# Optimization experiments

Measured on AMD Instinct MI355X. Metric: run time of the kernel, lower is better.

The kernel has to match this reference:

```python
import jax, jax.numpy as jnp
import numpy as np

DIM = 1024
SEQ_LEN = 4096
K_RANK = 256
HEADS = 16
HEAD_DIM = DIM // HEADS
BATCH = 4


def setup_inputs() -> dict:
    key = jax.random.key(0)
    k1, k2, k3, k4 = jax.random.split(key, 4)
    x = jax.random.normal(k1, (BATCH, SEQ_LEN, DIM), dtype=jnp.float32)
    W_qkv = jax.random.normal(k2, (DIM, 3 * DIM), dtype=jnp.float32) * (DIM ** -0.5)
    E = jax.random.normal(k3, (SEQ_LEN, K_RANK), dtype=jnp.float32)
    W_out = jax.random.normal(k4, (DIM, DIM), dtype=jnp.float32) * (DIM ** -0.5)
    b_out = jnp.zeros((DIM,), dtype=jnp.float32)
    return {"x": x, "W_qkv": W_qkv, "E": E, "W_out": W_out, "b_out": b_out}


def reference(x, W_qkv, E, W_out, b_out):
    B, N, D = x.shape
    scale = HEAD_DIM ** -0.5
    qkv = x @ W_qkv                                    # [B, N, 3D]
    q, k, v = jnp.split(qkv, 3, axis=-1)
    # [B, N, D] -> [B, H, N, hd]
    reshape_heads = lambda t: t.reshape(B, N, HEADS, HEAD_DIM).transpose(0, 2, 1, 3)
    q, k, v = map(reshape_heads, (q, k, v))
    # Linformer low-rank projection along sequence: [B, H, N, hd] -> [B, H, k, hd]
    k_proj = jnp.einsum('bhnd,nk->bhkd', k, E)
    v_proj = jnp.einsum('bhnd,nk->bhkd', v, E)
    scores = jnp.einsum('bhnd,bhkd->bhnk', q, k_proj) * scale  # [B, H, N, k]
    attn = jax.nn.softmax(scores, axis=-1)
    out = jnp.einsum('bhnk,bhkd->bhnd', attn, v_proj)  # [B, H, N, hd]
    out = out.transpose(0, 2, 1, 3).reshape(B, N, D)
    return out @ W_out + b_out
```

## Files before the change

### kernel.cpp

```cpp
#include <hip/hip_runtime.h>
#include <hip/hip_bf16.h>

typedef _Float16 f16;
typedef __attribute__((ext_vector_type(4))) _Float16 f16x4;
typedef __attribute__((ext_vector_type(8))) _Float16 f16x8;
typedef __attribute__((ext_vector_type(4))) float f32x4;

#define DIM 1024
#define SEQ 4096
#define KRNK 256
#define NH 16
#define HD 64
#define NB 4
#define ROWS (NB*SEQ)
#define NSPLIT 4

typedef const void __attribute__((address_space(1))) as1cv;
typedef void __attribute__((address_space(3))) as3v;

static __device__ __forceinline__ void glds16(const void* g, void* l) {
  __builtin_amdgcn_global_load_lds((as1cv*)g, (as3v*)l, 16, 0, 0);
}

template<int MODE>
__global__ __launch_bounds__(256) void k_prep_w(const float* __restrict__ in,
                                                f16* __restrict__ oh, f16* __restrict__ ol,
                                                int R, int C) {
  __shared__ float tile[64][65];
  int rtiles = R >> 6;
  int rt = blockIdx.x % rtiles, ct = blockIdx.x / rtiles;
  int r0 = rt << 6, c0 = ct << 6, t = threadIdx.x;
#pragma unroll
  for (int i = 0; i < 16; ++i) {
    int e = t + i * 256; int r = e >> 6, c = e & 63;
    tile[r][c] = in[(size_t)(r0 + r) * C + c0 + c];
  }
  __syncthreads();
#pragma unroll
  for (int i = 0; i < 16; ++i) {
    int e = t + i * 256; int c = e >> 6, r = e & 63;
    float v = tile[r][c];
    size_t idx = (size_t)(c0 + c) * R + r0 + r;
    if constexpr (MODE == 0) {
      v *= 256.0f;
      f16 h = (f16)v;
      oh[idx] = h;
      ol[idx] = (f16)(v - (float)h);
    } else {
      oh[idx] = (f16)v;
    }
  }
}

template<bool WH>
__global__ __launch_bounds__(256) void k_tsplit(const float* __restrict__ in,
                                                f16* __restrict__ oh,
                                                f16* __restrict__ oth,
                                                int R, int C) {
  __shared__ float tile[64][65];
  int rtiles = R >> 6;
  int rt = blockIdx.x % rtiles, ct = blockIdx.x / rtiles;
  int r0 = rt << 6, c0 = ct << 6, t = threadIdx.x;
  int cq = (t & 15) * 4, rr = t >> 4;
#pragma unroll
  for (int i = 0; i < 4; ++i) {
    int r = rr + i * 16;
    f32x4 v = *(const f32x4*)&in[(size_t)(r0 + r) * C + c0 + cq];
    tile[r][cq] = v[0]; tile[r][cq + 1] = v[1];
    tile[r][cq + 2] = v[2]; tile[r][cq + 3] = v[3];
    if constexpr (WH) {
      f16x4 h = {(f16)v[0], (f16)v[1], (f16)v[2], (f16)v[3]};
      *(f16x4*)&oh[(size_t)(r0 + r) * C + c0 + cq] = h;
    }
  }
  __syncthreads();
  int d4 = (t >> 4) * 4, sq = (t & 15) * 4;
#pragma unroll
  for (int j = 0; j < 4; ++j) {
    f16x4 h4;
#pragma unroll
    for (int k = 0; k < 4; ++k) h4[k] = (f16)tile[sq + k][d4 + j];
    *(f16x4*)&oth[(size_t)(c0 + d4 + j) * R + r0 + sq] = h4;
  }
}

template<bool ASPL, bool BSPL, int MT, int NT>
static __device__ __forceinline__ void mm_core(
    const f16* __restrict__ Ah, const f16* __restrict__ Al, int lda,
    const f16* __restrict__ Bh, const f16* __restrict__ Bl, int ldb,
    int bm, int bn, int K,
    f16* sAh, f16* sAl, f16* sBh, f16* sBl,
    f32x4 (&acc)[MT / 32][NT / 32]) {
  constexpr int MREP = MT / 32, NREP = NT / 32;
  constexpr int AI = MT / 32, BI = NT / 32;
  const int t = threadIdx.x;
  const int lane = t & 63, w = t >> 6;
  const int wr = w >> 1, wc = w & 1;
  const int l15 = lane & 15, hi = lane >> 4;
  const f32x4 zero = {0.f, 0.f, 0.f, 0.f};
#pragma unroll
  for (int m = 0; m < MREP; ++m)
#pragma unroll
    for (int n = 0; n < NREP; ++n) acc[m][n] = zero;

  for (int kk = 0; kk < K; kk += 64) {
#pragma unroll
    for (int i = 0; i < AI; ++i) {
      int c = t + i * 256;
      int row = c >> 3, cc = c & 7;
      size_t g = (size_t)(bm + row) * lda + kk + ((cc ^ (row & 7)) * 8);
      glds16(Ah + g, &sAh[c * 8]);
      if constexpr (ASPL) glds16(Al + g, &sAl[c * 8]);
    }
#pragma unroll
    for (int i = 0; i < BI; ++i) {
      int c = t + i * 256;
      int row = c >> 3, cc = c & 7;
      size_t g = (size_t)(bn + row) * ldb + kk + ((cc ^ (row & 7)) * 8);
      glds16(Bh + g, &sBh[c * 8]);
      if constexpr (BSPL) glds16(Bl + g, &sBl[c * 8]);
    }
    __syncthreads();

    f16x8 avh[MREP][2], avl[MREP][2], bvh[NREP][2], bvl[NREP][2];
#pragma unroll
    for (int m = 0; m < MREP; ++m)
#pragma unroll
      for (int ks = 0; ks < 2; ++ks) {
        int R = wr * (MT / 2) + m * 16 + l15;
        int off = R * 64 + (((ks * 4 + hi) ^ (R & 7)) * 8);
        avh[m][ks] = *(const f16x8*)&sAh[off];
        if constexpr (ASPL) avl[m][ks] = *(const f16x8*)&sAl[off];
      }
#pragma unroll
    for (int n = 0; n < NREP; ++n)
#pragma unroll
      for (int ks = 0; ks < 2; ++ks) {
        int R = wc * (NT / 2) + n * 16 + l15;
        int off = R * 64 + (((ks * 4 + hi) ^ (R & 7)) * 8);
        bvh[n][ks] = *(const f16x8*)&sBh[off];
        if constexpr (BSPL) bvl[n][ks] = *(const f16x8*)&sBl[off];
      }
#pragma unroll
    for (int m = 0; m < MREP; ++m)
#pragma unroll
      for (int n = 0; n < NREP; ++n)
#pragma unroll
        for (int ks = 0; ks < 2; ++ks) {
          if constexpr (ASPL && BSPL) {
            acc[m][n] = __builtin_amdgcn_mfma_f32_16x16x32_f16(avl[m][ks], bvh[n][ks], acc[m][n], 0, 0, 0);
            acc[m][n] = __builtin_amdgcn_mfma_f32_16x16x32_f16(avh[m][ks], bvl[n][ks], acc[m][n], 0, 0, 0);
          } else if constexpr (BSPL) {
            acc[m][n] = __builtin_amdgcn_mfma_f32_16x16x32_f16(avh[m][ks], bvl[n][ks], acc[m][n], 0, 0, 0);
          }
          acc[m][n] = __builtin_amdgcn_mfma_f32_16x16x32_f16(avh[m][ks], bvh[n][ks], acc[m][n], 0, 0, 0);
        }
    __syncthreads();
  }
}

__global__ __launch_bounds__(256) void k_xe2(const f16* __restrict__ Eth,
                                             const f16* __restrict__ xth,
                                             float* __restrict__ XEp) {
  __shared__ __align__(16) f16 sA[128 * 64];
  __shared__ __align__(16) f16 sB[64 * 64];
  int bx = blockIdx.x;
  int nt = bx & 15, mt = (bx >> 4) & 1, b = (bx >> 5) & 3, sp = bx >> 7;
  int bm = mt << 7, bn = nt << 6;
  int koff = sp * (SEQ / NSPLIT);
  f32x4 acc[4][2];
  mm_core<false, false, 128, 64>(Eth + koff, nullptr, SEQ,
                                 xth + (size_t)b * SEQ + koff, nullptr, ROWS,
                                 bm, bn, SEQ / NSPLIT, sA, nullptr, sB, nullptr, acc);
  const int t = threadIdx.x, lane = t & 63, w = t >> 6;
  const int wr = w >> 1, wc = w & 1, l15 = lane & 15, hi = lane >> 4;
#pragma unroll
  for (int m = 0; m < 4; ++m)
#pragma unroll
    for (int n = 0; n < 2; ++n)
#pragma unroll
      for (int r = 0; r < 4; ++r) {
        int kr = bm + wr * 64 + m * 16 + hi * 4 + r;
        int dd = bn + wc * 32 + n * 16 + l15;
        XEp[(((size_t)sp * NB + b) * KRNK + kr) * DIM + dd] = acc[m][n][r];
      }
}

__global__ __launch_bounds__(256) void k_xered(const float* __restrict__ XEp,
                                               f16* __restrict__ XEh,
                                               f16* __restrict__ XEl) {
  size_t i = (size_t)blockIdx.x * 256 + threadIdx.x;
  const size_t sstride = (size_t)NB * KRNK * DIM / 4;
  const f32x4* p = (const f32x4*)XEp;
  f32x4 s = p[i];
#pragma unroll
  for (int sp = 1; sp < NSPLIT; ++sp) s += p[i + sp * sstride];
  f16x4 h4, l4;
#pragma unroll
  for (int j = 0; j < 4; ++j) {
    f16 h = (f16)s[j];
    h4[j] = h;
    l4[j] = (f16)(s[j] - (float)h);
  }
  *(f16x4*)&XEh[i * 4] = h4;
  *(f16x4*)&XEl[i * 4] = l4;
}

__global__ __launch_bounds__(256) void k_gq(const f16* __restrict__ xh,
                                            const f16* __restrict__ Wph,
                                            f16* __restrict__ q) {
  __shared__ __align__(16) f16 sA[64 * 64];
  __shared__ __align__(16) f16 sB[128 * 64];
  int bx = blockIdx.x;
  int mt = bx & 255, nt = bx >> 8;
  int bm = mt << 6, bn = nt << 7;
  f32x4 acc[2][4];
  mm_core<false, false, 64, 128>(xh, nullptr, DIM, Wph, nullptr, DIM, bm, bn, DIM,
                                 sA, nullptr, sB, nullptr, acc);
  const int t = threadIdx.x, lane = t & 63, w = t >> 6;
  const int wr = w >> 1, wc = w & 1, l15 = lane & 15, hi = lane >> 4;
#pragma unroll
  for (int m = 0; m < 2; ++m)
#pragma unroll
    for (int n = 0; n < 4; ++n)
#pragma unroll
      for (int r = 0; r < 4; ++r) {
        int row = bm + wr * 32 + m * 16 + hi * 4 + r;
        int col = bn + wc * 64 + n * 16 + l15;
        q[(size_t)row * DIM + col] = (f16)(acc[m][n][r] * (1.0f / 256.0f));
      }
}

__global__ __launch_bounds__(256) void k_t2(const f16* __restrict__ XEh,
                                            const f16* __restrict__ XEl,
                                            const f16* __restrict__ Wph,
                                            const f16* __restrict__ Wpl,
                                            f16* __restrict__ kph,
                                            f16* __restrict__ vpt) {
  __shared__ __align__(16) f16 sAh[128 * 64], sAl[128 * 64];
  __shared__ __align__(16) f16 sBh[64 * 64], sBl[64 * 64];
  int bx = blockIdx.x;
  int nt = bx & 15, mt = (bx >> 4) & 1, b = (bx >> 5) & 3, kv = bx >> 7;
  size_t abase = (size_t)b * KRNK * DIM;
  size_t wbase = (size_t)(DIM + kv * DIM) * DIM;
  f32x4 acc[4][2];
  mm_core<true, true, 128, 64>(XEh + abase, XEl + abase, DIM, Wph + wbase, Wpl + wbase, DIM,
                               mt << 7, nt << 6, DIM, sAh, sAl, sBh, sBl, acc);
  const int t = threadIdx.x, lane = t & 63, w = t >> 6;
  const int wr = w >> 1, wc = w & 1, l15 = lane & 15, hi = lane >> 4;
#pragma unroll
  for (int m = 0; m < 4; ++m)
#pragma unroll
    for (int n = 0; n < 2; ++n)
#pragma unroll
      for (int r = 0; r < 4; ++r) {
        int row = (mt << 7) + wr * 64 + m * 16 + hi * 4 + r;
        int col = (nt << 6) + wc * 32 + n * 16 + l15;
        float s = acc[m][n][r] * (1.0f / 256.0f);
        if (!kv) kph[((size_t)(b * KRNK + row)) * DIM + col] = (f16)s;
        else     vpt[((size_t)(b * DIM + col)) * KRNK + row] = (f16)s;
      }
}

__global__ __launch_bounds__(256) void k_attn(const f16* __restrict__ q,
                                              const f16* __restrict__ kph,
                                              const f16* __restrict__ vpt,
                                              f16* __restrict__ oattn) {
  __shared__ __align__(16) f16 sBuf[2][64 * 64];
  __shared__ __align__(16) f16 sP[64 * KRNK];
  int bx0 = blockIdx.x;
  int swz = (bx0 & 7) * 512 + (bx0 >> 3);
  int qb = swz & 63;
  int bh = swz >> 6;
  int b = bh >> 4, h = bh & 15;
  int t = threadIdx.x;
  int lane = t & 63, w = t >> 6;
  int l15 = lane & 15, hi = lane >> 4;

  const f16* kbase = kph + ((size_t)(b * KRNK)) * DIM + h * HD;
  const f16* vbase = vpt + ((size_t)(b * DIM + h * HD)) * KRNK;

  auto stageK = [&](int c, int bufi) {
#pragma unroll
    for (int i = 0; i < 2; ++i) {
      int sid = w * 128 + i * 64 + lane;
      int kr = sid >> 3, sl = sid & 7;
      glds16(kbase + (size_t)(c * 64 + kr) * DIM + ((sl ^ (kr & 7)) * 8),
             &sBuf[bufi][sid * 8]);
    }
  };
  auto stageV = [&](int c, int bufi) {
#pragma unroll
    for (int i = 0; i < 2; ++i) {
      int sid = w * 128 + i * 64 + lane;
      int hd = sid >> 3, sl = sid & 7;
      glds16(vbase + (size_t)hd * KRNK + c * 64 + ((sl ^ (hd & 7)) * 8),
             &sBuf[bufi][sid * 8]);
    }
  };

  int seqrow = qb * 64 + w * 16 + l15;
  const f16* qg = q + ((size_t)(b * SEQ + seqrow)) * DIM + h * HD;
  f16x8 aq[2];
  aq[0] = *(const f16x8*)(qg + hi * 8);
  aq[1] = *(const f16x8*)(qg + 32 + hi * 8);

  const f32x4 zero = {0.f, 0.f, 0.f, 0.f};
  f32x4 s[16];

  stageK(0, 0);
#pragma unroll
  for (int c = 0; c < 4; ++c) {
    __syncthreads();
    if (c < 3) stageK(c + 1, (c + 1) & 1);
    else       stageV(0, 0);
#pragma unroll
    for (int n = 0; n < 4; ++n) {
      int nn = c * 4 + n;
      s[nn] = zero;
      int krl = n * 16 + l15;
#pragma unroll
      for (int ks = 0; ks < 2; ++ks) {
        f16x8 bk = *(const f16x8*)&sBuf[c & 1][krl * 64 + (((ks * 4 + hi) ^ (krl & 7)) * 8)];
        s[nn] = __builtin_amdgcn_mfma_f32_16x16x32_f16(bk, aq[ks], s[nn], 0, 0, 0);
      }
    }
  }

  const float scale = 0.125f;
  float m0 = s[0][0];
#pragma unroll
  for (int n = 0; n < 16; ++n)
#pragma unroll
    for (int r = 0; r < 4; ++r) m0 = fmaxf(m0, s[n][r]);
  m0 = fmaxf(m0, __shfl_xor(m0, 16));
  m0 = fmaxf(m0, __shfl_xor(m0, 32));
  float sm0 = 0.f, sm1 = 0.f, sm2 = 0.f, sm3 = 0.f;
#pragma unroll
  for (int n = 0; n < 16; ++n) {
    float p0 = __expf((s[n][0] - m0) * scale);
    float p1 = __expf((s[n][1] - m0) * scale);
    float p2 = __expf((s[n][2] - m0) * scale);
    float p3 = __expf((s[n][3] - m0) * scale);
    s[n][0] = p0; s[n][1] = p1; s[n][2] = p2; s[n][3] = p3;
    sm0 += p0; sm1 += p1; sm2 += p2; sm3 += p3;
  }
  float sm = (sm0 + sm1) + (sm2 + sm3);
  sm += __shfl_xor(sm, 16);
  sm += __shfl_xor(sm, 32);
  float inv = 1.0f / sm;

  {
    int qrow = w * 16 + l15;
    int qm = qrow & 7;
    f16* rowp = &sP[qrow * KRNK];
#pragma unroll
    for (int n = 0; n < 16; ++n) {
      int chunk = 2 * n + (hi >> 1);
      f16x4 pv = {(f16)s[n][0], (f16)s[n][1], (f16)s[n][2], (f16)s[n][3]};
      *(f16x4*)&rowp[((chunk ^ qm) * 8) + (hi & 1) * 4] = pv;
    }
  }

  f32x4 o[4];
#pragma unroll
  for (int n = 0; n < 4; ++n) o[n] = zero;
  int qloc = w * 16 + l15;
#pragma unroll
  for (int c = 0; c < 4; ++c) {
    __syncthreads();
    if (c < 3) stageV(c + 1, (c + 1) & 1);
#pragma unroll
    for (int sub = 0; sub < 2; ++sub) {
      int chunk = c * 8 + sub * 4 + hi;
      f16x8 pa = *(const f16x8*)&sP[qloc * KRNK + ((chunk ^ (qloc & 7)) * 8)];
#pragma unroll
      for (int n = 0; n < 4; ++n) {
        int hd = n * 16 + l15;
        f16x8 bv = *(const f16x8*)&sBuf[c & 1][hd * 64 + (((sub * 4 + hi) ^ (hd & 7)) * 8)];
        o[n] = __builtin_amdgcn_mfma_f32_16x16x32_f16(pa, bv, o[n], 0, 0, 0);
      }
    }
  }

  float invr[4];
#pragma unroll
  for (int r = 0; r < 4; ++r) invr[r] = __shfl(inv, hi * 4 + r);

  size_t obase = ((size_t)(b * SEQ + qb * 64)) * DIM + h * HD;
#pragma unroll
  for (int n = 0; n < 4; ++n)
#pragma unroll
    for (int r = 0; r < 4; ++r) {
      int qloc2 = w * 16 + hi * 4 + r;
      int hd = n * 16 + l15;
      oattn[obase + (size_t)qloc2 * DIM + hd] = (f16)(o[n][r] * invr[r]);
    }
}

__global__ __launch_bounds__(256) void k_go(const f16* __restrict__ oattn,
                                            const f16* __restrict__ WoT,
                                            const float* __restrict__ bias,
                                            float* __restrict__ out) {
  __shared__ __align__(16) f16 sA[128 * 64];
  __shared__ __align__(16) f16 sB[128 * 64];
  int bx = blockIdx.x;
  int mt = bx & 127, nt = bx >> 7;
  int bm = mt << 7, bn = nt << 7;
  f32x4 acc[4][4];
  mm_core<false, false, 128, 128>(oattn, nullptr, DIM, WoT, nullptr, DIM, bm, bn, DIM,
                                  sA, nullptr, sB, nullptr, acc);
  const int t = threadIdx.x, lane = t & 63, w = t >> 6;
  const int wr = w >> 1, wc = w & 1, l15 = lane & 15, hi = lane >> 4;
#pragma unroll
  for (int m = 0; m < 4; ++m)
#pragma unroll
    for (int n = 0; n < 4; ++n)
#pragma unroll
      for (int r = 0; r < 4; ++r) {
        int row = bm + wr * 64 + m * 16 + hi * 4 + r;
        int col = bn + wc * 64 + n * 16 + l15;
        out[(size_t)row * DIM + col] = acc[m][n][r] + bias[col];
      }
}

extern "C" void kernel_launch(void* const* d_in, const int* in_sizes, int n_in,
                              void* d_out, int out_size, void* d_ws, size_t ws_size,
                              hipStream_t stream) {
  const float* x    = (const float*)d_in[0];
  const float* Wqkv = (const float*)d_in[1];
  const float* E    = (const float*)d_in[2];
  const float* Wout = (const float*)d_in[3];
  const float* bout = (const float*)d_in[4];
  float* out = (float*)d_out;

  char* p = (char*)d_ws;
  f16* Wph = (f16*)p;  p += (size_t)2 * 3 * DIM * DIM;
  f16* Wpl = (f16*)p;  p += (size_t)2 * 3 * DIM * DIM;
  f16* WoT = (f16*)p;  p += (size_t)2 * DIM * DIM;
  f16* xh  = (f16*)p;  p += (size_t)2 * ROWS * DIM;
  f16* xth = (f16*)p;  p += (size_t)2 * DIM * ROWS;
  f16* Eth = (f16*)p;  p += (size_t)2 * KRNK * SEQ;
  f16* XEh = (f16*)p;  p += (size_t)2 * NB * KRNK * DIM;
  f16* XEl = (f16*)p;  p += (size_t)2 * NB * KRNK * DIM;
  f16* kph = (f16*)p;  p += (size_t)2 * NB * KRNK * DIM;
  f16* vpt = (f16*)p;  p += (size_t)2 * NB * DIM * KRNK;
  f16* oattn = (f16*)p; p += (size_t)2 * ROWS * DIM;
  float* XEp = (float*)p;  p += (size_t)4 * NSPLIT * NB * KRNK * DIM;
  size_t need = (size_t)(p - (char*)d_ws);
  if (ws_size < need) return;

  f16* q = xth;

  k_prep_w<0><<<(DIM / 64) * (3 * DIM / 64), 256, 0, stream>>>(Wqkv, Wph, Wpl, DIM, 3 * DIM);
  k_prep_w<1><<<(DIM / 64) * (DIM / 64), 256, 0, stream>>>(Wout, WoT, nullptr, DIM, DIM);
  k_tsplit<true><<<(ROWS / 64) * (DIM / 64), 256, 0, stream>>>(x, xh, xth, ROWS, DIM);
  k_tsplit<false><<<(SEQ / 64) * (KRNK / 64), 256, 0, stream>>>(E, nullptr, Eth, SEQ, KRNK);
  k_xe2<<<512, 256, 0, stream>>>(Eth, xth, XEp);
  k_xered<<<(NB * KRNK * DIM / 4) / 256, 256, 0, stream>>>(XEp, XEh, XEl);
  k_gq<<<2048, 256, 0, stream>>>(xh, Wph, q);
  k_t2<<<256, 256, 0, stream>>>(XEh, XEl, Wph, Wpl, kph, vpt);
  k_attn<<<64 * 64, 256, 0, stream>>>(q, kph, vpt, oattn);
  k_go<<<1024, 256, 0, stream>>>(oattn, WoT, bout, out);
}
```

Before: 227.2 us.

## Double-buffer LDS tiles in shared GEMM core to overlap loads with MFMA

The shared mm_core GEMM loop now uses two LDS buffers: the next K-tile is issued through global_load_lds while the current tile is consumed. A partial s_waitcnt vmcnt plus a raw s_barrier replaces the full __syncthreads. This hides global-load latency behind the MFMA work, at the cost of doubling LDS per block, which can lower occupancy (the t2 kernel goes to 96KB). The vmcnt count relies on each glds16 counting as exactly one outstanding load per thread.

Measured after the change: 230.3 us. Within noise of the previous version (+1.3%).

```diff
diff --git a/kernel.cpp b/kernel.cpp
--- a/kernel.cpp
+++ b/kernel.cpp
@@ -93,6 +93,8 @@
     f32x4 (&acc)[MT / 32][NT / 32]) {
   constexpr int MREP = MT / 32, NREP = NT / 32;
   constexpr int AI = MT / 32, BI = NT / 32;
+  constexpr int ASZ = MT * 64, BSZ = NT * 64;
+  constexpr int LPS = AI * (ASPL ? 2 : 1) + BI * (BSPL ? 2 : 1);
   const int t = threadIdx.x;
   const int lane = t & 63, w = t >> 6;
   const int wr = w >> 1, wc = w & 1;
@@ -103,24 +105,36 @@
 #pragma unroll
     for (int n = 0; n < NREP; ++n) acc[m][n] = zero;
 
-  for (int kk = 0; kk < K; kk += 64) {
+  auto stage = [&](int kk, int bufi) {
 #pragma unroll
     for (int i = 0; i < AI; ++i) {
       int c = t + i * 256;
       int row = c >> 3, cc = c & 7;
       size_t g = (size_t)(bm + row) * lda + kk + ((cc ^ (row & 7)) * 8);
-      glds16(Ah + g, &sAh[c * 8]);
-      if constexpr (ASPL) glds16(Al + g, &sAl[c * 8]);
+      glds16(Ah + g, &sAh[bufi * ASZ + c * 8]);
+      if constexpr (ASPL) glds16(Al + g, &sAl[bufi * ASZ + c * 8]);
     }
 #pragma unroll
     for (int i = 0; i < BI; ++i) {
       int c = t + i * 256;
       int row = c >> 3, cc = c & 7;
       size_t g = (size_t)(bn + row) * ldb + kk + ((cc ^ (row & 7)) * 8);
-      glds16(Bh + g, &sBh[c * 8]);
-      if constexpr (BSPL) glds16(Bl + g, &sBl[c * 8]);
-    }
-    __syncthreads();
+      glds16(Bh + g, &sBh[bufi * BSZ + c * 8]);
+      if constexpr (BSPL) glds16(Bl + g, &sBl[bufi * BSZ + c * 8]);
+    }
+  };
+
+  const int nsteps = K >> 6;
+  stage(0, 0);
+  for (int ki = 0; ki < nsteps; ++ki) {
+    const int cur = ki & 1;
+    if (ki + 1 < nsteps) {
+      stage((ki + 1) << 6, cur ^ 1);
+      asm volatile("s_waitcnt vmcnt(%0)" :: "n"(LPS) : "memory");
+    } else {
+      asm volatile("s_waitcnt vmcnt(0)" ::: "memory");
+    }
+    __builtin_amdgcn_s_barrier();
 
     f16x8 avh[MREP][2], avl[MREP][2], bvh[NREP][2], bvl[NREP][2];
 #pragma unroll
@@ -128,7 +142,7 @@
 #pragma unroll
       for (int ks = 0; ks < 2; ++ks) {
         int R = wr * (MT / 2) + m * 16 + l15;
-        int off = R * 64 + (((ks * 4 + hi) ^ (R & 7)) * 8);
+        int off = cur * ASZ + R * 64 + (((ks * 4 + hi) ^ (R & 7)) * 8);
         avh[m][ks] = *(const f16x8*)&sAh[off];
         if constexpr (ASPL) avl[m][ks] = *(const f16x8*)&sAl[off];
       }
@@ -137,7 +151,7 @@
 #pragma unroll
       for (int ks = 0; ks < 2; ++ks) {
         int R = wc * (NT / 2) + n * 16 + l15;
-        int off = R * 64 + (((ks * 4 + hi) ^ (R & 7)) * 8);
+        int off = cur * BSZ + R * 64 + (((ks * 4 + hi) ^ (R & 7)) * 8);
         bvh[n][ks] = *(const f16x8*)&sBh[off];
         if constexpr (BSPL) bvl[n][ks] = *(const f16x8*)&sBl[off];
       }
@@ -155,15 +169,15 @@
           }
           acc[m][n] = __builtin_amdgcn_mfma_f32_16x16x32_f16(avh[m][ks], bvh[n][ks], acc[m][n], 0, 0, 0);
         }
-    __syncthreads();
+    __builtin_amdgcn_s_barrier();
   }
 }
 
 __global__ __launch_bounds__(256) void k_xe2(const f16* __restrict__ Eth,
                                              const f16* __restrict__ xth,
                                              float* __restrict__ XEp) {
-  __shared__ __align__(16) f16 sA[128 * 64];
-  __shared__ __align__(16) f16 sB[64 * 64];
+  __shared__ __align__(16) f16 sA[2 * 128 * 64];
+  __shared__ __align__(16) f16 sB[2 * 64 * 64];
   int bx = blockIdx.x;
   int nt = bx & 15, mt = (bx >> 4) & 1, b = (bx >> 5) & 3, sp = bx >> 7;
   int bm = mt << 7, bn = nt << 6;
@@ -209,8 +223,8 @@
 __global__ __launch_bounds__(256) void k_gq(const f16* __restrict__ xh,
                                             const f16* __restrict__ Wph,
                                             f16* __restrict__ q) {
-  __shared__ __align__(16) f16 sA[64 * 64];
-  __shared__ __align__(16) f16 sB[128 * 64];
+  __shared__ __align__(16) f16 sA[2 * 64 * 64];
+  __shared__ __align__(16) f16 sB[2 * 128 * 64];
   int bx = blockIdx.x;
   int mt = bx & 255, nt = bx >> 8;
   int bm = mt << 6, bn = nt << 7;
@@ -237,8 +251,8 @@
                                             const f16* __restrict__ Wpl,
                                             f16* __restrict__ kph,
                                             f16* __restrict__ vpt) {
-  __shared__ __align__(16) f16 sAh[128 * 64], sAl[128 * 64];
-  __shared__ __align__(16) f16 sBh[64 * 64], sBl[64 * 64];
+  __shared__ __align__(16) f16 sAh[2 * 128 * 64], sAl[2 * 128 * 64];
+  __shared__ __align__(16) f16 sBh[2 * 64 * 64], sBl[2 * 64 * 64];
   int bx = blockIdx.x;
   int nt = bx & 15, mt = (bx >> 4) & 1, b = (bx >> 5) & 3, kv = bx >> 7;
   size_t abase = (size_t)b * KRNK * DIM;
@@ -402,8 +416,8 @@
                                             const f16* __restrict__ WoT,
                                             const float* __restrict__ bias,
                                             float* __restrict__ out) {
-  __shared__ __align__(16) f16 sA[128 * 64];
-  __shared__ __align__(16) f16 sB[128 * 64];
+  __shared__ __align__(16) f16 sA[2 * 128 * 64];
+  __shared__ __align__(16) f16 sB[2 * 128 * 64];
   int bx = blockIdx.x;
   int mt = bx & 127, nt = bx >> 7;
   int bm = mt << 7, bn = nt << 7;
```
